# Kernel optimization log

Hardware: AMD Instinct MI355X
Metric: run time of the kernel (lower is better)

## Reference

```python
import jax, jax.numpy as jnp
import numpy as np

NT = 100000   # total word nodes (B graphs * N nodes)
B = 50        # number of graphs in the batch
E = 1600000   # total edges
V = 15000     # vocab (num_word)
D_IN = 128    # h_inp
D_H = 128     # h_dim


def setup_inputs() -> dict:
    key = jax.random.key(0)
    ks = jax.random.split(key, 12)
    return {
        "node_ids": jax.random.randint(ks[0], (NT,), 0, V),
        "src": jax.random.randint(ks[1], (E,), 0, NT),
        "dst": jax.random.randint(ks[2], (E,), 0, NT),
        "edge_weight": jax.random.uniform(ks[3], (E,), dtype=jnp.float32),
        "y_data": jax.random.uniform(ks[4], (B,), dtype=jnp.float32),
        "word_embeds": jax.random.normal(ks[5], (V, D_IN), dtype=jnp.float32) * 0.1,
        "W1": jax.random.normal(ks[6], (D_IN, D_H), dtype=jnp.float32) * 0.05,
        "b1": jax.random.normal(ks[7], (D_H,), dtype=jnp.float32) * 0.05,
        "W2": jax.random.normal(ks[8], (D_H, D_H), dtype=jnp.float32) * 0.05,
        "b2": jax.random.normal(ks[9], (D_H,), dtype=jnp.float32) * 0.05,
        "W_out": jax.random.normal(ks[10], (D_H, 1), dtype=jnp.float32) * 0.05,
        "b_out": jax.random.normal(ks[11], (1,), dtype=jnp.float32) * 0.05,
    }


def _word_graph_layer(h, W, b, src, dst, edge_weight, deg):
    # Linear projection, then DGL u_mul_e + mean aggregation over incoming edges.
    Wh = h @ W + b                                   # [NT, D]
    m = Wh[src] * edge_weight[:, None]               # gather + edge-weight mul, [E, D]
    s = jax.ops.segment_sum(m, dst, num_segments=NT)  # scatter-add, [NT, D]
    # mean over incoming messages; nodes with no in-edges keep 0 (DGL semantics)
    return jnp.where(deg[:, None] > 0, s / jnp.maximum(deg, 1.0)[:, None], 0.0)


def reference(node_ids, src, dst, edge_weight, y_data, word_embeds,
              W1, b1, W2, b2, W_out, b_out):
    deg = jax.ops.segment_sum(jnp.ones_like(edge_weight), dst, num_segments=NT)
    h = word_embeds[node_ids]                        # [NT, D_IN]
    h = _word_graph_layer(h, W1, b1, src, dst, edge_weight, deg)
    h = jax.nn.leaky_relu(h, negative_slope=0.01)
    h = _word_graph_layer(h, W2, b2, src, dst, edge_weight, deg)
    # per-graph mean pool; equal graph sizes so padded mean == true mean
    word_pool = h.reshape(B, NT // B, D_H).mean(axis=1)   # [B, D_H]
    logits = (word_pool @ W_out + b_out).reshape(-1)      # [B]
    # binary_cross_entropy_with_logits, mean reduction (numerically stable)
    loss = jnp.mean(jnp.maximum(logits, 0.0) - logits * y_data
                    + jnp.log1p(jnp.exp(-jnp.abs(logits))))
    y_pred = jax.nn.sigmoid(logits)[:, None]              # [B, 1]
    return (loss, y_pred)
```

## Files before the change

### kernel.cpp

```cpp
#include <hip/hip_runtime.h>
#include <hip/hip_fp16.h>
#include <math.h>

#define NT 100000
#define B_GRAPHS 50
#define NE 1600000
#define V 15000
#define D 128
#define NODES_PER_GRAPH (NT / B_GRAPHS)

#define POOL_N (B_GRAPHS * D + B_GRAPHS)

#define BSH 8
#define BIN_DSTS 256
#define NBIN ((NT + BIN_DSTS - 1) / BIN_DSTS)
#define SLACK (3 * BIN_DSTS)
#define EPB 4096
#define NFB ((NE + EPB - 1) / EPB)
#define BUF_SORT 5632
#define STAGE_STRIDE 4608
#define PAY_STRIDE (STAGE_STRIDE + SLACK)
#define PAY_TAIL 512
#define PR 16
#define PROJ_BLOCKS ((V + PR - 1) / PR)

__device__ __forceinline__ unsigned enc2_e5m2(float a, float b) {
  unsigned ha = __half_as_ushort(__float2half(a));
  unsigned hb = __half_as_ushort(__float2half(b));
  ha = ((ha + 0x7fu + ((ha >> 8) & 1u)) >> 8) & 0xffu;
  hb = ((hb + 0x7fu + ((hb >> 8) & 1u)) >> 8) & 0xffu;
  return ha | (hb << 8);
}
__device__ __forceinline__ unsigned enc4_e5m2(float a, float b, float c, float d) {
  return enc2_e5m2(a, b) | (enc2_e5m2(c, d) << 16);
}

template<bool USE_WID>
__device__ __forceinline__ int pick_idx(const int4& q, int half) {
  int lo = USE_WID ? (q.x & 0xffff) : q.y;
  int hi = USE_WID ? (q.z & 0xffff) : q.w;
  return half ? hi : lo;
}
__device__ __forceinline__ void consume2h(const int4& q, unsigned v, int half,
                                          __half2& A01, __half2& A23, __half2& SW) {
  unsigned wm = (unsigned)(half ? q.z : q.x);
  unsigned wd = (wm >> 16) | (wm & 0xffff0000u);
  unsigned hp0 = ((v & 0xffu) << 8) | ((v & 0xff00u) << 16);
  unsigned hp1 = ((v >> 8) & 0xff00u) | (v & 0xff000000u);
  __half2 w2 = *(__half2*)&wd;
  A01 = __hfma2(w2, *(__half2*)&hp0, A01);
  A23 = __hfma2(w2, *(__half2*)&hp1, A23);
  SW = __hadd2(SW, w2);
}
__device__ __forceinline__ void consume2h_ns(const int4& q, unsigned v, int half,
                                             __half2& A01, __half2& A23) {
  unsigned wm = (unsigned)(half ? q.z : q.x);
  unsigned wd = (wm >> 16) | (wm & 0xffff0000u);
  unsigned hp0 = ((v & 0xffu) << 8) | ((v & 0xff00u) << 16);
  unsigned hp1 = ((v >> 8) & 0xff00u) | (v & 0xff000000u);
  __half2 w2 = *(__half2*)&wd;
  A01 = __hfma2(w2, *(__half2*)&hp0, A01);
  A23 = __hfma2(w2, *(__half2*)&hp1, A23);
}
__device__ __forceinline__ int4 ld2s(const int2* bp, int i) {
  int2 a = bp[i], c = bp[i + 1];
  return make_int4(a.x, a.y, c.x, c.y);
}

__global__ __launch_bounds__(512)
void k_pb(const float* __restrict__ embeds, const float* __restrict__ W1,
          const float* __restrict__ b1, unsigned* __restrict__ P1p8,
          float* __restrict__ pool, int2* __restrict__ payTail,
          const int* __restrict__ src, const int* __restrict__ dst,
          const float* __restrict__ ew, const int* __restrict__ node_ids,
          int* __restrict__ binCursor, int2* __restrict__ stage) {
  __shared__ union {
    struct {
      int h[512], sc[512], gbase[512], cur[512];
      int wsum[8], woff[8];
      unsigned short binOf[EPB];
      int2 buf[EPB];
    } f;
    struct {
      float sE[PR][D];
      float sO[PR][D];
    } p;
  } U;
  int t = threadIdx.x;
  if (blockIdx.x < NFB) {
    int lane = t & 63, wv = t >> 6;
    U.f.h[t] = 0;
    __syncthreads();
    int base = blockIdx.x * EPB;
    int d_[EPB / 512], b_[EPB / 512];
#pragma unroll
    for (int i = 0; i < EPB / 512; ++i) {
      int e = base + i * 512 + t;
      int d = (e < NE) ? dst[e] : -1;
      d_[i] = d;
      b_[i] = (d >= 0) ? (d >> BSH) : -1;
      if (d >= 0) atomicAdd(&U.f.h[b_[i]], 1);
    }
    __syncthreads();
    int c = U.f.h[t];
    int v = c;
#pragma unroll
    for (int off = 1; off < 64; off <<= 1) {
      int x = __shfl_up(v, off);
      if (lane >= off) v += x;
    }
    if (lane == 63) U.f.wsum[wv] = v;
    __syncthreads();
    if (t == 0) {
      int a = 0;
#pragma unroll
      for (int i = 0; i < 8; ++i) { U.f.woff[i] = a; a += U.f.wsum[i]; }
    }
    __syncthreads();
    int incl = v + U.f.woff[wv];
    U.f.sc[t] = incl;
    U.f.cur[t] = incl - c;
    if (t < NBIN && c > 0) U.f.gbase[t] = atomicAdd(&binCursor[t], c);
    __syncthreads();
    int total = U.f.sc[511];
#pragma unroll
    for (int i = 0; i < EPB / 512; ++i) {
      int e = base + i * 512 + t;
      if (e < NE) {
        int s = src[e];
        unsigned uw = __float_as_uint(ew[e]);
        unsigned wb = (uw + 0x7fffu + ((uw >> 16) & 1u)) & 0xffff0000u;
        int wid = node_ids[s];
        int dl = d_[i] & (BIN_DSTS - 1);
        int p = atomicAdd(&U.f.cur[b_[i]], 1);
        U.f.buf[p] = make_int2((int)(wb | (unsigned)wid), s | (dl << 17));
        U.f.binOf[p] = (unsigned short)b_[i];
      }
    }
    __syncthreads();
    for (int i = t; i < total; i += 512) {
      int b = U.f.binOf[i];
      int local = i - (U.f.sc[b] - U.f.h[b]);
      stage[(size_t)b * STAGE_STRIDE + U.f.gbase[b] + local] = U.f.buf[i];
    }
  } else {
    int pb = blockIdx.x - NFB;
    if (pb == 0) {
      for (int i = t; i < POOL_N; i += 512) pool[i] = 0.f;
      for (int i = t; i < PAY_TAIL; i += 512) payTail[i] = make_int2(0, 0);
    }
    int row0 = pb * PR;
    for (int i = t; i < PR * D; i += 512) {
      int r = i >> 7, c = i & 127;
      int vv = row0 + r;
      U.p.sE[r][c] = (vv < V) ? embeds[(size_t)vv * D + c] : 0.f;
    }
    __syncthreads();
    int c = t & 127, rg = (t >> 7) * 4;
    float bd = b1[c];
    float acc[4];
#pragma unroll
    for (int r = 0; r < 4; ++r) acc[r] = bd;
#pragma unroll 4
    for (int k = 0; k < D; ++k) {
      float w = W1[k * D + c];
#pragma unroll
      for (int r = 0; r < 4; ++r) acc[r] = fmaf(U.p.sE[rg + r][k], w, acc[r]);
    }
#pragma unroll
    for (int r = 0; r < 4; ++r) U.p.sO[rg + r][c] = acc[r];
    __syncthreads();
    {
      int r = t >> 5, li = t & 31;
      int vv = row0 + r;
      if (vv < V)
        P1p8[(size_t)vv * 32 + li] =
            enc4_e5m2(U.p.sO[r][4 * li], U.p.sO[r][4 * li + 1],
                      U.p.sO[r][4 * li + 2], U.p.sO[r][4 * li + 3]);
    }
  }
}

__global__ __launch_bounds__(512)
void k_sortagg(const int2* __restrict__ stage, const int* __restrict__ binCnt,
               const unsigned* __restrict__ P1p8,
               int* __restrict__ rowD, int* __restrict__ cntD,
               int2* __restrict__ pay, unsigned* __restrict__ h1p8) {
  __shared__ int h2[BIN_DSTS], cur2[BIN_DSTS], offArr[BIN_DSTS];
  __shared__ float invD[BIN_DSTS];
  __shared__ int wsum4[4], woff4[4];
  __shared__ int sh_end;
  __shared__ int2 buf[BUF_SORT];
  int b = blockIdx.x, t = threadIdx.x;
  int lane = t & 63, wv = t >> 6;
  int cnt = binCnt[b];
  int sb = b * STAGE_STRIDE;
  int pbase = b * PAY_STRIDE;
  int dst0 = b << BSH;
  if (t < BIN_DSTS) h2[t] = 0;
  __syncthreads();
  for (int i = t; i < cnt; i += 512)
    atomicAdd(&h2[(stage[sb + i].y >> 17) & 255], 1);
  __syncthreads();
  int c = (t < BIN_DSTS) ? h2[t] : 0;
  int pc = (c + 3) & ~3;
  int v = (t < BIN_DSTS) ? pc : 0;
#pragma unroll
  for (int off = 1; off < 64; off <<= 1) {
    int x = __shfl_up(v, off);
    if (lane >= off) v += x;
  }
  if (lane == 63 && wv < 4) wsum4[wv] = v;
  __syncthreads();
  if (t == 0) {
    int a = 0;
#pragma unroll
    for (int i = 0; i < 4; ++i) { woff4[i] = a; a += wsum4[i]; }
    sh_end = a;
  }
  __syncthreads();
  if (t < BIN_DSTS) {
    int myoff = v + woff4[wv] - pc;
    invD[t] = (c > 0) ? (1.0f / (float)c) : 0.0f;
    cur2[t] = myoff;
    offArr[t] = myoff;
    int n = dst0 + t;
    if (n < NT) { rowD[n] = pbase + myoff; cntD[n] = c; }
  }
  __syncthreads();
  int end = sh_end + 24;
  if (end > PAY_STRIDE) end = PAY_STRIDE;
  for (int i = t; i < end; i += 512) buf[i] = make_int2(0, 0);
  __syncthreads();
  for (int i = t; i < cnt; i += 512) {
    int2 r = stage[sb + i];
    int dl = (r.y >> 17) & 255;
    float w = __uint_as_float((unsigned)r.x & 0xffff0000u);
    float wp = w * invD[dl];
    unsigned wh = (unsigned)__half_as_ushort(__float2half(wp));
    int p = atomicAdd(&cur2[dl], 1);
    buf[p] = make_int2((int)((wh << 16) | ((unsigned)r.x & 0xffffu)), r.y & 0x1ffff);
  }
  __syncthreads();
  for (int i = t; i < end; i += 512) pay[pbase + i] = buf[i];
  int li = lane & 31, half = lane >> 5;
  for (int j = 0; j < 32; ++j) {
    int dl = wv * 32 + j;
    int beg = offArr[dl];
    int cn = h2[dl];
    int G = (cn + 3) >> 2;
    __half2 A01 = __half2half2(__float2half(0.f));
    __half2 A23 = A01;
    int4 qa0 = ld2s(buf, beg + 0), qb0 = ld2s(buf, beg + 2);
    int4 qa1 = ld2s(buf, beg + 4), qb1 = ld2s(buf, beg + 6);
    unsigned va0 = P1p8[(size_t)pick_idx<true>(qa0, half) * 32 + li];
    unsigned vb0 = P1p8[(size_t)pick_idx<true>(qb0, half) * 32 + li];
    unsigned va1 = P1p8[(size_t)pick_idx<true>(qa1, half) * 32 + li];
    unsigned vb1 = P1p8[(size_t)pick_idx<true>(qb1, half) * 32 + li];
    for (int g = 0; g < G; ++g) {
      int4 qa2 = ld2s(buf, beg + 4 * g + 8);
      int4 qb2 = ld2s(buf, beg + 4 * g + 10);
      unsigned vn0 = P1p8[(size_t)pick_idx<true>(qa2, half) * 32 + li];
      unsigned vn1 = P1p8[(size_t)pick_idx<true>(qb2, half) * 32 + li];
      consume2h_ns(qa0, va0, half, A01, A23);
      consume2h_ns(qb0, vb0, half, A01, A23);
      qa0 = qa1; qb0 = qb1; qa1 = qa2; qb1 = qb2;
      va0 = va1; vb0 = vb1; va1 = vn0; vb1 = vn1;
    }
    float2 f01 = __half22float2(A01);
    float2 f23 = __half22float2(A23);
    float a0 = f01.x, a1 = f01.y, a2 = f23.x, a3 = f23.y;
    a0 += __shfl_down(a0, 32);
    a1 += __shfl_down(a1, 32);
    a2 += __shfl_down(a2, 32);
    a3 += __shfl_down(a3, 32);
    if (lane < 32) {
      int n = dst0 + dl;
      if (n < NT) {
        float x0 = a0, x1 = a1, x2 = a2, x3 = a3;
        x0 = (x0 > 0.f) ? x0 : 0.01f * x0;
        x1 = (x1 > 0.f) ? x1 : 0.01f * x1;
        x2 = (x2 > 0.f) ? x2 : 0.01f * x2;
        x3 = (x3 > 0.f) ? x3 : 0.01f * x3;
        h1p8[(size_t)n * 32 + li] = enc4_e5m2(x0, x1, x2, x3);
      }
    }
  }
}

__device__ __forceinline__ void gather_row_g(const int2* __restrict__ pay,
                                             const unsigned* __restrict__ tab,
                                             int beg, int cnt, int li, int half,
                                             __half2& A01, __half2& A23, __half2& SW) {
  int G = (cnt + 3) >> 2;
  const int4* __restrict__ pp = (const int4*)(pay + beg);
  int4 q0a = pp[0], q0b = pp[1];
  int4 q1a = pp[2], q1b = pp[3];
  int4 q2a = pp[4], q2b = pp[5];
  int4 q3a = pp[6], q3b = pp[7];
  int4 q4a = pp[8], q4b = pp[9];
  unsigned va0 = tab[(size_t)pick_idx<false>(q0a, half) * 32 + li];
  unsigned vb0 = tab[(size_t)pick_idx<false>(q0b, half) * 32 + li];
  unsigned va1 = tab[(size_t)pick_idx<false>(q1a, half) * 32 + li];
  unsigned vb1 = tab[(size_t)pick_idx<false>(q1b, half) * 32 + li];
  unsigned va2 = tab[(size_t)pick_idx<false>(q2a, half) * 32 + li];
  unsigned vb2 = tab[(size_t)pick_idx<false>(q2b, half) * 32 + li];
  for (int g = 0; g < G; ++g) {
    unsigned vn0 = tab[(size_t)pick_idx<false>(q3a, half) * 32 + li];
    unsigned vn1 = tab[(size_t)pick_idx<false>(q3b, half) * 32 + li];
    int4 qna = pp[2 * g + 10];
    int4 qnb = pp[2 * g + 11];
    consume2h(q0a, va0, half, A01, A23, SW);
    consume2h(q0b, vb0, half, A01, A23, SW);
    q0a = q1a; q0b = q1b; q1a = q2a; q1b = q2b; q2a = q3a; q2b = q3b;
    q3a = q4a; q3b = q4b; q4a = qna; q4b = qnb;
    va0 = va1; vb0 = vb1; va1 = va2; vb1 = vb2; va2 = vn0; vb2 = vn1;
  }
}

#define NPW2 10
#define BLKS_PER_G (NODES_PER_GRAPH / (4 * NPW2))
__global__ void k_agg2(const int2* __restrict__ pay,
                       const int* __restrict__ rowD, const int* __restrict__ cntD,
                       const unsigned* __restrict__ h1p8,
                       float* __restrict__ pool) {
  int g = blockIdx.x / BLKS_PER_G;
  int chunk = blockIdx.x % BLKS_PER_G;
  int w = threadIdx.x >> 6, lane = threadIdx.x & 63;
  int li = lane & 31, half = lane >> 5;
  int nbase = g * NODES_PER_GRAPH + chunk * (4 * NPW2) + w * NPW2;
  __half2 A01 = __half2half2(__float2half(0.f));
  __half2 A23 = A01, SW = A01;
  for (int i = 0; i < NPW2; ++i) {
    int n = nbase + i;
    int beg = __builtin_amdgcn_readfirstlane(rowD[n]);
    int cnt = __builtin_amdgcn_readfirstlane(cntD[n]);
    gather_row_g(pay, h1p8, beg, cnt, li, half, A01, A23, SW);
  }
  float2 f01 = __half22float2(A01);
  float2 f23 = __half22float2(A23);
  float s0 = f01.x, s1 = f01.y, s2 = f23.x, s3 = f23.y;
  float sc = __low2float(SW);
  s0 += __shfl_down(s0, 32);
  s1 += __shfl_down(s1, 32);
  s2 += __shfl_down(s2, 32);
  s3 += __shfl_down(s3, 32);
  sc += __shfl_down(sc, 32);
  __shared__ float sS[4 * 128];
  __shared__ float sC[4];
  if (lane < 32) {
    sS[w * 128 + 4 * li + 0] = s0;
    sS[w * 128 + 4 * li + 1] = s1;
    sS[w * 128 + 4 * li + 2] = s2;
    sS[w * 128 + 4 * li + 3] = s3;
  }
  if (lane == 0) sC[w] = sc;
  __syncthreads();
  int t = threadIdx.x;
  if (t < 128) {
    float v = sS[t] + sS[128 + t] + sS[256 + t] + sS[384 + t];
    atomicAdd(&pool[g * D + t], v);
  }
  if (t == 0) atomicAdd(&pool[B_GRAPHS * D + g], sC[0] + sC[1] + sC[2] + sC[3]);
}

__global__ void k_final(const float* __restrict__ poolS, const float* __restrict__ poolC,
                        const float* __restrict__ W2, const float* __restrict__ b2,
                        const float* __restrict__ W_out, const float* __restrict__ b_out,
                        const float* __restrict__ y, float* __restrict__ out) {
  __shared__ float w2o[D];
  __shared__ float s2oArr[D];
  __shared__ float s2o_sh;
  __shared__ float logits[64];
  int t = threadIdx.x;
  int w = t >> 6, lane = t & 63;
  if (t < D) {
    float acc = 0.f;
    for (int d = 0; d < D; ++d) acc = fmaf(W2[t * D + d], W_out[d], acc);
    w2o[t] = acc;
  } else {
    int j = t - D;
    s2oArr[j] = b2[j] * W_out[j];
  }
  __syncthreads();
  if (t < 64) {
    float v = s2oArr[lane] + s2oArr[64 + lane];
#pragma unroll
    for (int off = 32; off > 0; off >>= 1) v += __shfl_down(v, off);
    if (lane == 0) s2o_sh = v;
  }
  __syncthreads();
  float s2o = s2o_sh;
  float bout = b_out[0];
  const float invN = 1.0f / (float)NODES_PER_GRAPH;
  for (int g = w; g < B_GRAPHS; g += 4) {
    float v = poolS[g * D + lane] * w2o[lane]
            + poolS[g * D + 64 + lane] * w2o[64 + lane];
#pragma unroll
    for (int off = 32; off > 0; off >>= 1) v += __shfl_down(v, off);
    if (lane == 0) {
      float l = v * invN + poolC[g] * invN * s2o + bout;
      logits[g] = l;
      out[1 + g] = 1.0f / (1.0f + expf(-l));
    }
  }
  __syncthreads();
  if (t < 64) {
    float term = 0.f;
    if (lane < B_GRAPHS) {
      float l = logits[lane];
      term = fmaxf(l, 0.f) - l * y[lane] + log1pf(expf(-fabsf(l)));
    }
#pragma unroll
    for (int off = 32; off > 0; off >>= 1) term += __shfl_down(term, off);
    if (lane == 0) out[0] = term / (float)B_GRAPHS;
  }
}

extern "C" void kernel_launch(void* const* d_in, const int* in_sizes, int n_in,
                              void* d_out, int out_size, void* d_ws, size_t ws_size,
                              hipStream_t stream) {
  const int*   node_ids = (const int*)d_in[0];
  const int*   src      = (const int*)d_in[1];
  const int*   dst      = (const int*)d_in[2];
  const float* ew       = (const float*)d_in[3];
  const float* y        = (const float*)d_in[4];
  const float* embeds   = (const float*)d_in[5];
  const float* W1       = (const float*)d_in[6];
  const float* b1       = (const float*)d_in[7];
  const float* W2       = (const float*)d_in[8];
  const float* b2       = (const float*)d_in[9];
  const float* W_out    = (const float*)d_in[10];
  const float* b_out    = (const float*)d_in[11];
  float* out = (float*)d_out;
  (void)in_sizes; (void)n_in; (void)out_size; (void)ws_size;

  char* ws = (char*)d_ws;
  size_t off = 0;
  auto alloc = [&](size_t bytes) {
    size_t r = off;
    off = (off + bytes + 511) & ~(size_t)511;
    return r;
  };
  size_t o_binCur = alloc(512 * 4);
  size_t o_pool   = alloc((size_t)POOL_N * 4);
  size_t o_rowD   = alloc((size_t)(NT + 1) * 4);
  size_t o_cntD   = alloc((size_t)NT * 4);
  size_t o_P1p8   = alloc((size_t)V * 32 * 4);
  size_t o_h1p8   = alloc((size_t)NT * 32 * 4);
  size_t o_stage  = alloc((size_t)NBIN * STAGE_STRIDE * 8);
  size_t o_pay    = alloc(((size_t)NBIN * PAY_STRIDE + PAY_TAIL) * 8);

  int*      binCursor= (int*)(ws + o_binCur);
  float*    pool     = (float*)(ws + o_pool);
  int*      rowD     = (int*)(ws + o_rowD);
  int*      cntD     = (int*)(ws + o_cntD);
  unsigned* P1p8     = (unsigned*)(ws + o_P1p8);
  unsigned* h1p8     = (unsigned*)(ws + o_h1p8);
  int2*     stage    = (int2*)(ws + o_stage);
  int2*     pay      = (int2*)(ws + o_pay);
  int2*     payTail  = pay + (size_t)NBIN * PAY_STRIDE;

  hipMemsetAsync(binCursor, 0, 512 * 4, stream);
  k_pb<<<NFB + PROJ_BLOCKS, 512, 0, stream>>>(embeds, W1, b1, P1p8, pool, payTail,
                                              src, dst, ew, node_ids, binCursor, stage);
  k_sortagg<<<NBIN, 512, 0, stream>>>(stage, binCursor, P1p8, rowD, cntD, pay, h1p8);
  k_agg2<<<B_GRAPHS * BLKS_PER_G, 256, 0, stream>>>(pay, rowD, cntD, h1p8, pool);
  k_final<<<1, 256, 0, stream>>>(pool, pool + B_GRAPHS * D, W2, b2, W_out, b_out, y, out);
}
```

Before: 255.7 us.

## Split fused bin-sort and layer-1 aggregation into separate sort and gather kernels

The fused sort-plus-aggregate kernel becomes two kernels. k_binsort only sorts edges per destination bin and writes the payload to global memory. A new k_agg1 then performs the layer-1 gather from the global payload with the deeper prefetch pipeline already used by layer 2. The goal is to raise occupancy and parallelism for the gather, since the fused kernel ran 391 blocks of 512 threads with large shared-memory use and each wave walked 32 rows serially. The cost is an extra launch and a global re-read of the payload that was previously served from LDS.

After: 253.7 us (median of 2 runs). About the same (-0.8%).

```diff
diff --git a/kernel.cpp b/kernel.cpp
--- a/kernel.cpp
+++ b/kernel.cpp
@@ -33,38 +33,6 @@
 }
 __device__ __forceinline__ unsigned enc4_e5m2(float a, float b, float c, float d) {
   return enc2_e5m2(a, b) | (enc2_e5m2(c, d) << 16);
-}
-
-template<bool USE_WID>
-__device__ __forceinline__ int pick_idx(const int4& q, int half) {
-  int lo = USE_WID ? (q.x & 0xffff) : q.y;
-  int hi = USE_WID ? (q.z & 0xffff) : q.w;
-  return half ? hi : lo;
-}
-__device__ __forceinline__ void consume2h(const int4& q, unsigned v, int half,
-                                          __half2& A01, __half2& A23, __half2& SW) {
-  unsigned wm = (unsigned)(half ? q.z : q.x);
-  unsigned wd = (wm >> 16) | (wm & 0xffff0000u);
-  unsigned hp0 = ((v & 0xffu) << 8) | ((v & 0xff00u) << 16);
-  unsigned hp1 = ((v >> 8) & 0xff00u) | (v & 0xff000000u);
-  __half2 w2 = *(__half2*)&wd;
-  A01 = __hfma2(w2, *(__half2*)&hp0, A01);
-  A23 = __hfma2(w2, *(__half2*)&hp1, A23);
-  SW = __hadd2(SW, w2);
-}
-__device__ __forceinline__ void consume2h_ns(const int4& q, unsigned v, int half,
-                                             __half2& A01, __half2& A23) {
-  unsigned wm = (unsigned)(half ? q.z : q.x);
-  unsigned wd = (wm >> 16) | (wm & 0xffff0000u);
-  unsigned hp0 = ((v & 0xffu) << 8) | ((v & 0xff00u) << 16);
-  unsigned hp1 = ((v >> 8) & 0xff00u) | (v & 0xff000000u);
-  __half2 w2 = *(__half2*)&wd;
-  A01 = __hfma2(w2, *(__half2*)&hp0, A01);
-  A23 = __hfma2(w2, *(__half2*)&hp1, A23);
-}
-__device__ __forceinline__ int4 ld2s(const int2* bp, int i) {
-  int2 a = bp[i], c = bp[i + 1];
-  return make_int4(a.x, a.y, c.x, c.y);
 }
 
 __global__ __launch_bounds__(512)
@@ -182,11 +150,10 @@
 }
 
 __global__ __launch_bounds__(512)
-void k_sortagg(const int2* __restrict__ stage, const int* __restrict__ binCnt,
-               const unsigned* __restrict__ P1p8,
+void k_binsort(const int2* __restrict__ stage, const int* __restrict__ binCnt,
                int* __restrict__ rowD, int* __restrict__ cntD,
-               int2* __restrict__ pay, unsigned* __restrict__ h1p8) {
-  __shared__ int h2[BIN_DSTS], cur2[BIN_DSTS], offArr[BIN_DSTS];
+               int2* __restrict__ pay) {
+  __shared__ int h2[BIN_DSTS], cur2[BIN_DSTS];
   __shared__ float invD[BIN_DSTS];
   __shared__ int wsum4[4], woff4[4];
   __shared__ int sh_end;
@@ -195,7 +162,7 @@
   int lane = t & 63, wv = t >> 6;
   int cnt = binCnt[b];
   int sb = b * STAGE_STRIDE;
-  int pbase = b * PAY_STRIDE;
+  int pb = b * PAY_STRIDE;
   int dst0 = b << BSH;
   if (t < BIN_DSTS) h2[t] = 0;
   __syncthreads();
@@ -223,9 +190,8 @@
     int myoff = v + woff4[wv] - pc;
     invD[t] = (c > 0) ? (1.0f / (float)c) : 0.0f;
     cur2[t] = myoff;
-    offArr[t] = myoff;
     int n = dst0 + t;
-    if (n < NT) { rowD[n] = pbase + myoff; cntD[n] = c; }
+    if (n < NT) { rowD[n] = pb + myoff; cntD[n] = c; }
   }
   __syncthreads();
   int end = sh_end + 24;
@@ -242,31 +208,73 @@
     buf[p] = make_int2((int)((wh << 16) | ((unsigned)r.x & 0xffffu)), r.y & 0x1ffff);
   }
   __syncthreads();
-  for (int i = t; i < end; i += 512) pay[pbase + i] = buf[i];
+  for (int i = t; i < end; i += 512) pay[pb + i] = buf[i];
+}
+
+template<bool USE_WID>
+__device__ __forceinline__ int pick_idx(const int4& q, int half) {
+  int lo = USE_WID ? (q.x & 0xffff) : q.y;
+  int hi = USE_WID ? (q.z & 0xffff) : q.w;
+  return half ? hi : lo;
+}
+__device__ __forceinline__ void consume2h(const int4& q, unsigned v, int half,
+                                          __half2& A01, __half2& A23, __half2& SW) {
+  unsigned wm = (unsigned)(half ? q.z : q.x);
+  unsigned wd = (wm >> 16) | (wm & 0xffff0000u);
+  unsigned hp0 = ((v & 0xffu) << 8) | ((v & 0xff00u) << 16);
+  unsigned hp1 = ((v >> 8) & 0xff00u) | (v & 0xff000000u);
+  __half2 w2 = *(__half2*)&wd;
+  A01 = __hfma2(w2, *(__half2*)&hp0, A01);
+  A23 = __hfma2(w2, *(__half2*)&hp1, A23);
+  SW = __hadd2(SW, w2);
+}
+
+template<bool USE_WID>
+__device__ __forceinline__ void gather_row(const int2* __restrict__ pay,
+                                           const unsigned* __restrict__ tab,
+                                           int beg, int cnt, int li, int half,
+                                           __half2& A01, __half2& A23, __half2& SW) {
+  int G = (cnt + 3) >> 2;
+  const int4* __restrict__ pp = (const int4*)(pay + beg);
+  int4 q0a = pp[0], q0b = pp[1];
+  int4 q1a = pp[2], q1b = pp[3];
+  int4 q2a = pp[4], q2b = pp[5];
+  int4 q3a = pp[6], q3b = pp[7];
+  int4 q4a = pp[8], q4b = pp[9];
+  unsigned va0 = tab[(size_t)pick_idx<USE_WID>(q0a, half) * 32 + li];
+  unsigned vb0 = tab[(size_t)pick_idx<USE_WID>(q0b, half) * 32 + li];
+  unsigned va1 = tab[(size_t)pick_idx<USE_WID>(q1a, half) * 32 + li];
+  unsigned vb1 = tab[(size_t)pick_idx<USE_WID>(q1b, half) * 32 + li];
+  unsigned va2 = tab[(size_t)pick_idx<USE_WID>(q2a, half) * 32 + li];
+  unsigned vb2 = tab[(size_t)pick_idx<USE_WID>(q2b, half) * 32 + li];
+  for (int g = 0; g < G; ++g) {
+    unsigned vn0 = tab[(size_t)pick_idx<USE_WID>(q3a, half) * 32 + li];
+    unsigned vn1 = tab[(size_t)pick_idx<USE_WID>(q3b, half) * 32 + li];
+    int4 qna = pp[2 * g + 10];
+    int4 qnb = pp[2 * g + 11];
+    consume2h(q0a, va0, half, A01, A23, SW);
+    consume2h(q0b, vb0, half, A01, A23, SW);
+    q0a = q1a; q0b = q1b; q1a = q2a; q1b = q2b; q2a = q3a; q2b = q3b;
+    q3a = q4a; q3b = q4b; q4a = qna; q4b = qnb;
+    va0 = va1; vb0 = vb1; va1 = va2; vb1 = vb2; va2 = vn0; vb2 = vn1;
+  }
+}
+
+#define NPW1 10
+__global__ void k_agg1(const int2* __restrict__ pay,
+                       const int* __restrict__ rowD, const int* __restrict__ cntD,
+                       const unsigned* __restrict__ P1p8,
+                       unsigned* __restrict__ h1p8) {
+  int w = threadIdx.x >> 6, lane = threadIdx.x & 63;
   int li = lane & 31, half = lane >> 5;
-  for (int j = 0; j < 32; ++j) {
-    int dl = wv * 32 + j;
-    int beg = offArr[dl];
-    int cn = h2[dl];
-    int G = (cn + 3) >> 2;
+  int nbase = blockIdx.x * (4 * NPW1) + w * NPW1;
+  for (int i = 0; i < NPW1; ++i) {
+    int n = nbase + i;
+    int beg = __builtin_amdgcn_readfirstlane(rowD[n]);
+    int cnt = __builtin_amdgcn_readfirstlane(cntD[n]);
     __half2 A01 = __half2half2(__float2half(0.f));
-    __half2 A23 = A01;
-    int4 qa0 = ld2s(buf, beg + 0), qb0 = ld2s(buf, beg + 2);
-    int4 qa1 = ld2s(buf, beg + 4), qb1 = ld2s(buf, beg + 6);
-    unsigned va0 = P1p8[(size_t)pick_idx<true>(qa0, half) * 32 + li];
-    unsigned vb0 = P1p8[(size_t)pick_idx<true>(qb0, half) * 32 + li];
-    unsigned va1 = P1p8[(size_t)pick_idx<true>(qa1, half) * 32 + li];
-    unsigned vb1 = P1p8[(size_t)pick_idx<true>(qb1, half) * 32 + li];
-    for (int g = 0; g < G; ++g) {
-      int4 qa2 = ld2s(buf, beg + 4 * g + 8);
-      int4 qb2 = ld2s(buf, beg + 4 * g + 10);
-      unsigned vn0 = P1p8[(size_t)pick_idx<true>(qa2, half) * 32 + li];
-      unsigned vn1 = P1p8[(size_t)pick_idx<true>(qb2, half) * 32 + li];
-      consume2h_ns(qa0, va0, half, A01, A23);
-      consume2h_ns(qb0, vb0, half, A01, A23);
-      qa0 = qa1; qb0 = qb1; qa1 = qa2; qb1 = qb2;
-      va0 = va1; vb0 = vb1; va1 = vn0; vb1 = vn1;
-    }
+    __half2 A23 = A01, SW = A01;
+    gather_row<true>(pay, P1p8, beg, cnt, li, half, A01, A23, SW);
     float2 f01 = __half22float2(A01);
     float2 f23 = __half22float2(A23);
     float a0 = f01.x, a1 = f01.y, a2 = f23.x, a3 = f23.y;
@@ -275,46 +283,13 @@
     a2 += __shfl_down(a2, 32);
     a3 += __shfl_down(a3, 32);
     if (lane < 32) {
-      int n = dst0 + dl;
-      if (n < NT) {
-        float x0 = a0, x1 = a1, x2 = a2, x3 = a3;
-        x0 = (x0 > 0.f) ? x0 : 0.01f * x0;
-        x1 = (x1 > 0.f) ? x1 : 0.01f * x1;
-        x2 = (x2 > 0.f) ? x2 : 0.01f * x2;
-        x3 = (x3 > 0.f) ? x3 : 0.01f * x3;
-        h1p8[(size_t)n * 32 + li] = enc4_e5m2(x0, x1, x2, x3);
-      }
-    }
-  }
-}
-
-__device__ __forceinline__ void gather_row_g(const int2* __restrict__ pay,
-                                             const unsigned* __restrict__ tab,
-                                             int beg, int cnt, int li, int half,
-                                             __half2& A01, __half2& A23, __half2& SW) {
-  int G = (cnt + 3) >> 2;
-  const int4* __restrict__ pp = (const int4*)(pay + beg);
-  int4 q0a = pp[0], q0b = pp[1];
-  int4 q1a = pp[2], q1b = pp[3];
-  int4 q2a = pp[4], q2b = pp[5];
-  int4 q3a = pp[6], q3b = pp[7];
-  int4 q4a = pp[8], q4b = pp[9];
-  unsigned va0 = tab[(size_t)pick_idx<false>(q0a, half) * 32 + li];
-  unsigned vb0 = tab[(size_t)pick_idx<false>(q0b, half) * 32 + li];
-  unsigned va1 = tab[(size_t)pick_idx<false>(q1a, half) * 32 + li];
-  unsigned vb1 = tab[(size_t)pick_idx<false>(q1b, half) * 32 + li];
-  unsigned va2 = tab[(size_t)pick_idx<false>(q2a, half) * 32 + li];
-  unsigned vb2 = tab[(size_t)pick_idx<false>(q2b, half) * 32 + li];
-  for (int g = 0; g < G; ++g) {
-    unsigned vn0 = tab[(size_t)pick_idx<false>(q3a, half) * 32 + li];
-    unsigned vn1 = tab[(size_t)pick_idx<false>(q3b, half) * 32 + li];
-    int4 qna = pp[2 * g + 10];
-    int4 qnb = pp[2 * g + 11];
-    consume2h(q0a, va0, half, A01, A23, SW);
-    consume2h(q0b, vb0, half, A01, A23, SW);
-    q0a = q1a; q0b = q1b; q1a = q2a; q1b = q2b; q2a = q3a; q2b = q3b;
-    q3a = q4a; q3b = q4b; q4a = qna; q4b = qnb;
-    va0 = va1; vb0 = vb1; va1 = va2; vb1 = vb2; va2 = vn0; vb2 = vn1;
+      float x0 = a0, x1 = a1, x2 = a2, x3 = a3;
+      x0 = (x0 > 0.f) ? x0 : 0.01f * x0;
+      x1 = (x1 > 0.f) ? x1 : 0.01f * x1;
+      x2 = (x2 > 0.f) ? x2 : 0.01f * x2;
+      x3 = (x3 > 0.f) ? x3 : 0.01f * x3;
+      h1p8[(size_t)n * 32 + li] = enc4_e5m2(x0, x1, x2, x3);
+    }
   }
 }
 
@@ -335,7 +310,7 @@
     int n = nbase + i;
     int beg = __builtin_amdgcn_readfirstlane(rowD[n]);
     int cnt = __builtin_amdgcn_readfirstlane(cntD[n]);
-    gather_row_g(pay, h1p8, beg, cnt, li, half, A01, A23, SW);
+    gather_row<false>(pay, h1p8, beg, cnt, li, half, A01, A23, SW);
   }
   float2 f01 = __half22float2(A01);
   float2 f23 = __half22float2(A23);
@@ -464,7 +439,8 @@
   hipMemsetAsync(binCursor, 0, 512 * 4, stream);
   k_pb<<<NFB + PROJ_BLOCKS, 512, 0, stream>>>(embeds, W1, b1, P1p8, pool, payTail,
                                               src, dst, ew, node_ids, binCursor, stage);
-  k_sortagg<<<NBIN, 512, 0, stream>>>(stage, binCursor, P1p8, rowD, cntD, pay, h1p8);
+  k_binsort<<<NBIN, 512, 0, stream>>>(stage, binCursor, rowD, cntD, pay);
+  k_agg1<<<NT / (4 * NPW1), 256, 0, stream>>>(pay, rowD, cntD, P1p8, h1p8);
   k_agg2<<<B_GRAPHS * BLKS_PER_G, 256, 0, stream>>>(pay, rowD, cntD, h1p8, pool);
   k_final<<<1, 256, 0, stream>>>(pool, pool + B_GRAPHS * D, W2, b2, W_out, b_out, y, out);
 }
```
